# Kernel optimization log

Hardware: AMD Instinct MI355X
Metric: run time of the kernel (lower is better)

Reference implementation:

```python
import jax, jax.numpy as jnp
import numpy as np

EPS = 1e-5
GROUPS = 32

def group_norm(x, w, b):
    B, C, H, W = x.shape
    g = GROUPS
    xr = x.reshape(B, g, C // g, H * W)
    mean = xr.mean(axis=(2, 3), keepdims=True)
    var = xr.var(axis=(2, 3), keepdims=True)
    h = ((xr - mean) / jnp.sqrt(var + EPS)).reshape(B, C, H, W)
    return h * w[None, :, None, None] + b[None, :, None, None]

def setup_inputs() -> dict:
    key = jax.random.key(0)
    ks = jax.random.split(key, 7)
    B, C, H, W = 8, 256, 64, 64
    d = C // 8  # 32
    x = jax.random.normal(ks[0], (B, C, H, W), dtype=jnp.float32)
    norm_w = 1.0 + 0.1 * jax.random.normal(ks[1], (C,), dtype=jnp.float32)
    norm_b = 0.1 * jax.random.normal(ks[2], (C,), dtype=jnp.float32)
    s = 1.0 / np.sqrt(C)
    Wq = jax.random.normal(ks[3], (d, C), dtype=jnp.float32) * s
    Wk = jax.random.normal(ks[4], (d, C), dtype=jnp.float32) * s
    Wv = jax.random.normal(ks[5], (C, C), dtype=jnp.float32) * s
    Wproj = jax.random.normal(ks[6], (C, C), dtype=jnp.float32) * s
    gamma = jnp.full((1,), 0.5, dtype=jnp.float32)  # torch init is 0; nonzero so attention path contributes
    return {"x": x, "norm_w": norm_w, "norm_b": norm_b, "Wq": Wq, "Wk": Wk,
            "Wv": Wv, "Wproj": Wproj, "gamma": gamma}

def reference(x, norm_w, norm_b, Wq, Wk, Wv, Wproj, gamma):
    B, C, H, W = x.shape
    N = H * W
    h = group_norm(x, norm_w, norm_b)           # (B,C,H,W)
    hf = h.reshape(B, C, N)                      # flatten spatial
    d = Wq.shape[0]
    q = jnp.einsum('dc,bcn->bnd', Wq, hf)        # (B,N,d)
    k = jnp.einsum('dc,bcn->bdn', Wk, hf)        # (B,d,N)
    v = jnp.einsum('oc,bcn->bno', Wv, hf)        # (B,N,C)
    scale = d ** (-0.5)
    attn = jax.nn.softmax(jnp.einsum('bnd,bdm->bnm', q, k) * scale, axis=-1)  # (B,N,N)
    out = jnp.einsum('bnm,bmo->bno', attn, v)    # (B,N,C)
    out = out.transpose(0, 2, 1).reshape(B, C, H, W)
    proj = jnp.einsum('oc,bchw->bohw', Wproj, out)
    return x + gamma[0] * proj
```

## Files before the change

kernel.cpp:

```cpp
#include <hip/hip_runtime.h>
#include <cstdint>


typedef __bf16 bf16x8 __attribute__((ext_vector_type(8)));
typedef float f32x4 __attribute__((ext_vector_type(4)));
typedef float f32x16 __attribute__((ext_vector_type(16)));
typedef unsigned int u32x4 __attribute__((ext_vector_type(4)));
typedef unsigned short u16x4 __attribute__((ext_vector_type(4)));
typedef unsigned short u16x8 __attribute__((ext_vector_type(8)));

#define DEVI __device__ __forceinline__

DEVI unsigned short f2bf(float f) {
    __bf16 h = (__bf16)f;
    return __builtin_bit_cast(unsigned short, h);
}
DEVI float bf2f(unsigned short u) {
    unsigned int x = ((unsigned int)u) << 16;
    return __builtin_bit_cast(float, x);
}

DEVI f32x4 mfma16(bf16x8 a, bf16x8 b, f32x4 c) {
    return __builtin_amdgcn_mfma_f32_16x16x32_bf16(a, b, c, 0, 0, 0);
}
DEVI f32x16 mfma32(bf16x8 a, bf16x8 b, f32x16 c) {
    return __builtin_amdgcn_mfma_f32_32x32x16_bf16(a, b, c, 0, 0, 0);
}

DEVI void glds16(const unsigned short* g, unsigned short* l) {
    const __attribute__((address_space(1))) unsigned int* gp =
        reinterpret_cast<const __attribute__((address_space(1))) unsigned int*>(
            reinterpret_cast<uintptr_t>(g));
    __attribute__((address_space(3))) unsigned int* lp =
        reinterpret_cast<__attribute__((address_space(3))) unsigned int*>(
            reinterpret_cast<uintptr_t>(l));
    __builtin_amdgcn_global_load_lds(gp, lp, 16, 0, 0);
}

DEVI void barrier_raw() {
    asm volatile("" ::: "memory");
    __builtin_amdgcn_s_barrier();
    asm volatile("" ::: "memory");
}
DEVI void wait_vm0() {
    __builtin_amdgcn_s_waitcnt(0x3F70);
}

#define QSCALE 0.2550663133f
#define MFIX   12.0f

__global__ __launch_bounds__(1024) void k_gnorm(
        const float* __restrict__ x, const float* __restrict__ gw,
        const float* __restrict__ gb, unsigned short* __restrict__ ht) {
    int bg = blockIdx.x;
    int b = bg >> 5, g = bg & 31;
    const float* xb = x + ((size_t)(b * 256 + g * 8)) * 4096;
    int t = threadIdx.x;
    int n0 = t * 4;
    f32x4 cv[8];
    #pragma unroll
    for (int c = 0; c < 8; c++) cv[c] = *(const f32x4*)(xb + c * 4096 + n0);
    float s1 = 0.f, s2 = 0.f;
    #pragma unroll
    for (int c = 0; c < 8; c++) {
        #pragma unroll
        for (int j = 0; j < 4; j++) { s1 += cv[c][j]; s2 += cv[c][j] * cv[c][j]; }
    }
    #pragma unroll
    for (int off = 1; off < 64; off <<= 1) {
        s1 += __shfl_xor(s1, off);
        s2 += __shfl_xor(s2, off);
    }
    __shared__ float red[34];
    int wv_ = t >> 6;
    if ((t & 63) == 0) { red[wv_ * 2] = s1; red[wv_ * 2 + 1] = s2; }
    __syncthreads();
    if (t == 0) {
        float a = 0.f, q = 0.f;
        #pragma unroll
        for (int i = 0; i < 16; i++) { a += red[i * 2]; q += red[i * 2 + 1]; }
        float mean = a * (1.f / 32768.f);
        float var = q * (1.f / 32768.f) - mean * mean;
        red[32] = mean; red[33] = rsqrtf(var + 1e-5f);
    }
    __syncthreads();
    float mean = red[32], rstd = red[33];
    float wv8[8], bv8[8];
    #pragma unroll
    for (int c = 0; c < 8; c++) { wv8[c] = gw[g * 8 + c] * rstd; bv8[c] = gb[g * 8 + c] - mean * rstd * gw[g * 8 + c]; }
    #pragma unroll
    for (int j = 0; j < 4; j++) {
        u16x8 pk;
        #pragma unroll
        for (int c = 0; c < 8; c++) pk[c] = f2bf(cv[c][j] * wv8[c] + bv8[c]);
        *(u16x8*)(&ht[((size_t)(b * 4096 + n0 + j)) * 256 + g * 8]) = pk;
    }
}

template <int EPI>
__global__ __launch_bounds__(256) void k_gemm(
        const unsigned short* __restrict__ A, void* __restrict__ outp,
        const float* __restrict__ xres, const float* __restrict__ gamma, int ldout,
        const float* __restrict__ wqf, const float* __restrict__ wkf,
        const float* __restrict__ wvf, void* __restrict__ outp2) {
    __shared__ unsigned short lA[128 * 72];
    __shared__ unsigned short lB[64 * 72];
    int t = threadIdx.x;
    int m0 = blockIdx.x * 128, n0 = blockIdx.y * 64;
    if (EPI == 3) {
        if (blockIdx.y == 0) n0 = 0;
        else n0 = (blockIdx.y - 1) * 64;
    }
    int w = t >> 6, lane = t & 63, l15 = lane & 15, quad = lane >> 4;
    f32x4 z4 = {0.f, 0.f, 0.f, 0.f};
    f32x4 acc[2][4];
    #pragma unroll
    for (int i = 0; i < 2; i++)
        #pragma unroll
        for (int j = 0; j < 4; j++) acc[i][j] = z4;

    auto ldB8 = [&](int row, int gc) -> u16x8 {
        const float* src;
        float sc = 1.f;
        if (EPI == 3) {
            if (blockIdx.y == 0) {
                if (row < 32) { src = wqf + (size_t)row * 256 + gc; sc = QSCALE; }
                else          { src = wkf + (size_t)(row - 32) * 256 + gc; }
            } else {
                src = wvf + (size_t)(n0 + row) * 256 + gc;
            }
        } else {
            src = wvf + (size_t)(n0 + row) * 256 + gc;
        }
        f32x4 a = *(const f32x4*)src;
        f32x4 b2 = *(const f32x4*)(src + 4);
        u16x8 r;
        #pragma unroll
        for (int j = 0; j < 4; j++) { r[j] = f2bf(a[j] * sc); r[4 + j] = f2bf(b2[j] * sc); }
        return r;
    };

    for (int kb = 0; kb < 4; kb++) {
        #pragma unroll
        for (int i = 0; i < 4; i++) {
            int ch = i * 256 + t;
            int row = ch >> 3, col = (ch & 7) * 8;
            u32x4 v = *(const u32x4*)(A + (size_t)(m0 + row) * 256 + kb * 64 + col);
            *(u32x4*)(&lA[row * 72 + col]) = v;
        }
        #pragma unroll
        for (int i = 0; i < 2; i++) {
            int ch = i * 256 + t;
            int row = ch >> 3, col = (ch & 7) * 8;
            u16x8 v = ldB8(row, kb * 64 + col);
            *(u16x8*)(&lB[row * 72 + col]) = v;
        }
        __syncthreads();
        #pragma unroll
        for (int ks = 0; ks < 2; ks++) {
            bf16x8 af[2], bfr[4];
            #pragma unroll
            for (int fr = 0; fr < 2; fr++)
                af[fr] = *(const bf16x8*)(&lA[(w * 32 + fr * 16 + l15) * 72 + ks * 32 + quad * 8]);
            #pragma unroll
            for (int fn = 0; fn < 4; fn++)
                bfr[fn] = *(const bf16x8*)(&lB[(fn * 16 + l15) * 72 + ks * 32 + quad * 8]);
            #pragma unroll
            for (int fr = 0; fr < 2; fr++)
                #pragma unroll
                for (int fn = 0; fn < 4; fn++)
                    acc[fr][fn] = mfma16(af[fr], bfr[fn], acc[fr][fn]);
        }
        __syncthreads();
    }

    bool epi0 = (EPI == 3 && blockIdx.y == 0);
    bool epi1 = (EPI == 3 && blockIdx.y != 0);
    if (epi0) {
        unsigned short* out = (unsigned short*)outp;
        #pragma unroll
        for (int fr = 0; fr < 2; fr++)
            #pragma unroll
            for (int fn = 0; fn < 4; fn++)
                #pragma unroll
                for (int r = 0; r < 4; r++) {
                    int m = m0 + w * 32 + fr * 16 + quad * 4 + r;
                    int n = n0 + fn * 16 + l15;
                    out[(size_t)m * ldout + n] = f2bf(acc[fr][fn][r]);
                }
    } else if (epi1) {
        unsigned short* out = (unsigned short*)outp2;
        int b = m0 >> 12, nb = (m0 & 4095) + w * 32;
        int swq = ((quad & 1) << 1) | (quad >> 1);
        #pragma unroll
        for (int fr = 0; fr < 2; fr++)
            #pragma unroll
            for (int fn = 0; fn < 4; fn++) {
                int o = n0 + fn * 16 + l15;
                int n = nb + fr * 16 + swq * 4;
                u16x4 pk;
                #pragma unroll
                for (int r = 0; r < 4; r++) pk[r] = f2bf(acc[fr][fn][r]);
                *(u16x4*)(&out[(((size_t)(b * 256 + o)) << 12) + n]) = pk;
            }
    } else {
        float* out = (float*)outp;
        float gm = gamma[0];
        int b = m0 >> 12, nb = (m0 & 4095) + w * 32;
        #pragma unroll
        for (int fr = 0; fr < 2; fr++)
            #pragma unroll
            for (int fn = 0; fn < 4; fn++) {
                int o = n0 + fn * 16 + l15;
                int n = nb + fr * 16 + quad * 4;
                size_t base = (((size_t)(b * 256 + o)) << 12) + n;
                f32x4 xv = *(const f32x4*)(xres + base);
                f32x4 ov;
                #pragma unroll
                for (int r = 0; r < 4; r++) ov[r] = xv[r] + gm * acc[fr][fn][r];
                *(f32x4*)(out + base) = ov;
            }
    }
}

__global__ __launch_bounds__(256, 2) void k_flash(
        const unsigned short* __restrict__ QK, const unsigned short* __restrict__ Vt,
        unsigned short* __restrict__ Oa) {
    __shared__ __align__(16) char smem[40960];
    int id = blockIdx.x;
    int b = id & 7;
    int r3 = id >> 3;
    int oh = r3 & 1, qblk = r3 >> 1;
    int t = threadIdx.x, w = t >> 6, ln = t & 63;
    int l31 = ln & 31, h = ln >> 5;
    int qh = w >> 1, kh = w & 1;
    int q0 = qblk * 128 + qh * 64;

    bf16x8 qb0[2], qb1[2];
    #pragma unroll
    for (int qt2 = 0; qt2 < 2; qt2++) {
        const unsigned short* qrow = QK + ((size_t)(b * 4096 + q0 + qt2 * 32 + l31)) * 64;
        qb0[qt2] = *(const bf16x8*)(qrow + h * 8);
        qb1[qt2] = *(const bf16x8*)(qrow + 16 + h * 8);
    }

    int cgK = (ln & 3) ^ ((ln >> 2) & 3) ^ ((ln >> 4) & 3);
    const unsigned short* gK = QK + ((size_t)(b * 4096 + w * 16 + (ln >> 2))) * 64 + 32 + cgK * 8;
    int vc8 = (ln & 7) ^ ((ln >> 3) & 7);
    const unsigned short* gV = Vt + (((size_t)(b * 256 + oh * 128 + w * 32 + (ln >> 3))) << 12) + vc8 * 8;

    unsigned short* lK0 = (unsigned short*)smem;
    unsigned short* lV0 = (unsigned short*)(smem + 4096);
    unsigned short* lK1 = (unsigned short*)(smem + 20480);
    unsigned short* lV1 = (unsigned short*)(smem + 24576);
    unsigned short* sK0 = lK0 + w * 512;
    unsigned short* sV0 = lV0 + w * 2048;
    unsigned short* sK1 = lK1 + w * 512;
    unsigned short* sV1 = lV1 + w * 2048;

    f32x16 z16;
    #pragma unroll
    for (int i = 0; i < 16; i++) z16[i] = 0.f;
    f32x16 minit;
    #pragma unroll
    for (int i = 0; i < 16; i++) minit[i] = -MFIX;
    f32x16 Oacc[2][4];
    #pragma unroll
    for (int qt2 = 0; qt2 < 2; qt2++)
        #pragma unroll
        for (int i = 0; i < 4; i++) Oacc[qt2][i] = z16;
    float lsum[2] = {0.f, 0.f};

    int gl = (l31 & 3) ^ ((l31 >> 2) & 3);
    const unsigned short* kf0p0 = lK0 + (kh * 32 + l31) * 32 + ((0 + h) ^ gl) * 8;
    const unsigned short* kf1p0 = lK0 + (kh * 32 + l31) * 32 + ((2 + h) ^ gl) * 8;
    const unsigned short* kf0p1 = lK1 + (kh * 32 + l31) * 32 + ((0 + h) ^ gl) * 8;
    const unsigned short* kf1p1 = lK1 + (kh * 32 + l31) * 32 + ((2 + h) ^ gl) * 8;
    int slotA = ((kh * 4 + 0 * 2 + h) ^ (ln & 7)) * 8;
    int slotB = ((kh * 4 + 1 * 2 + h) ^ (ln & 7)) * 8;

    auto stage = [&](int kn, unsigned short* sK, unsigned short* sV) {
        glds16(gK + (size_t)kn * 4096, sK);
        #pragma unroll
        for (int j = 0; j < 4; j++)
            glds16(gV + ((size_t)j * 8 << 12) + kn * 64, sV + j * 512);
    };

    auto compute = [&](const unsigned short* kf0p, const unsigned short* kf1p,
                       const unsigned short* lV) {
        bf16x8 kf0 = *(const bf16x8*)kf0p;
        bf16x8 kf1 = *(const bf16x8*)kf1p;
        bf16x8 pa[2][2];
        #pragma unroll
        for (int qt2 = 0; qt2 < 2; qt2++) {
            f32x16 St = mfma32(kf0, qb0[qt2], minit);
            St = mfma32(kf1, qb1[qt2], St);
            u16x8 p0u, p1u;
            float s = 0.f;
            #pragma unroll
            for (int j = 0; j < 8; j++) {
                float e0 = __builtin_amdgcn_exp2f(St[j]);
                float e1 = __builtin_amdgcn_exp2f(St[8 + j]);
                s += e0 + e1;
                p0u[j] = f2bf(e0);
                p1u[j] = f2bf(e1);
            }
            lsum[qt2] += s;
            pa[qt2][0] = __builtin_bit_cast(bf16x8, p0u);
            pa[qt2][1] = __builtin_bit_cast(bf16x8, p1u);
        }
        __builtin_amdgcn_s_setprio(1);
        #pragma unroll
        for (int nt = 0; nt < 4; nt++) {
            bf16x8 vf = *(const bf16x8*)(lV + (nt * 32 + l31) * 64 + slotA);
            Oacc[0][nt] = mfma32(pa[0][0], vf, Oacc[0][nt]);
            Oacc[1][nt] = mfma32(pa[1][0], vf, Oacc[1][nt]);
        }
        #pragma unroll
        for (int nt = 0; nt < 4; nt++) {
            bf16x8 vf = *(const bf16x8*)(lV + (nt * 32 + l31) * 64 + slotB);
            Oacc[0][nt] = mfma32(pa[0][1], vf, Oacc[0][nt]);
            Oacc[1][nt] = mfma32(pa[1][1], vf, Oacc[1][nt]);
        }
        __builtin_amdgcn_s_setprio(0);
    };

    stage(0, sK0, sV0);
    for (int kt = 0; kt < 64; kt += 2) {
        wait_vm0();
        barrier_raw();
        stage(kt + 1, sK1, sV1);
        compute(kf0p0, kf1p0, lV0);
        wait_vm0();
        barrier_raw();
        if (kt + 2 < 64) stage(kt + 2, sK0, sV0);
        compute(kf0p1, kf1p1, lV1);
    }
    #pragma unroll
    for (int qt2 = 0; qt2 < 2; qt2++) lsum[qt2] += __shfl_xor(lsum[qt2], 32);
    __syncthreads();

    float* sf = (float*)smem;
    int lbase = (kh ? 8192 : 8320) + qh * 64 + l31;
    sf[lbase] = lsum[0];
    sf[lbase + 32] = lsum[1];
    if (kh == 1) {
        #pragma unroll
        for (int qt2 = 0; qt2 < 2; qt2++)
            #pragma unroll
            for (int nt = 0; nt < 4; nt++)
                #pragma unroll
                for (int rg = 0; rg < 2; rg++) {
                    u16x8 pk;
                    #pragma unroll
                    for (int j = 0; j < 8; j++) pk[j] = f2bf(Oacc[qt2][nt][rg * 8 + j]);
                    *(u16x8*)(smem + qh * 16384 + qt2 * 8192 + nt * 2048 + rg * 1024 + ln * 16) = pk;
                }
    }
    __syncthreads();
    if (kh == 0) {
        #pragma unroll
        for (int qt2 = 0; qt2 < 2; qt2++) {
            float rl[16];
            #pragma unroll
            for (int r = 0; r < 16; r++) {
                int row = (r & 3) + 8 * (r >> 2) + 4 * h;
                float l = sf[8192 + qh * 64 + qt2 * 32 + row] +
                          sf[8320 + qh * 64 + qt2 * 32 + row];
                rl[r] = 1.f / l;
            }
            size_t rb = (size_t)(b * 4096 + qblk * 128 + qh * 64 + qt2 * 32);
            #pragma unroll
            for (int nt = 0; nt < 4; nt++)
                #pragma unroll
                for (int rg = 0; rg < 2; rg++) {
                    u16x8 pk = *(const u16x8*)(smem + qh * 16384 + qt2 * 8192 + nt * 2048 + rg * 1024 + ln * 16);
                    #pragma unroll
                    for (int j = 0; j < 8; j++) {
                        int r = rg * 8 + j;
                        float val = (Oacc[qt2][nt][r] + bf2f(pk[j])) * rl[r];
                        int row = (r & 3) + 8 * (r >> 2) + 4 * h;
                        Oa[(rb + row) * 256 + oh * 128 + nt * 32 + l31] = f2bf(val);
                    }
                }
        }
    }
}

extern "C" void kernel_launch(void* const* d_in, const int* in_sizes, int n_in,
                              void* d_out, int out_size, void* d_ws, size_t ws_size,
                              hipStream_t stream) {
    const float* x  = (const float*)d_in[0];
    const float* nw = (const float*)d_in[1];
    const float* nb = (const float*)d_in[2];
    const float* wq = (const float*)d_in[3];
    const float* wk = (const float*)d_in[4];
    const float* wv = (const float*)d_in[5];
    const float* wp = (const float*)d_in[6];
    const float* gm = (const float*)d_in[7];

    char* p = (char*)d_ws;
    unsigned short* ht  = (unsigned short*)p; p += (size_t)32768 * 256 * 2;
    unsigned short* qk  = (unsigned short*)p; p += (size_t)32768 * 64 * 2;
    unsigned short* vt  = (unsigned short*)p; p += (size_t)8 * 256 * 4096 * 2;
    unsigned short* oa  = (unsigned short*)p; p += (size_t)32768 * 256 * 2;

    k_gnorm<<<dim3(256), dim3(1024), 0, stream>>>(x, nw, nb, ht);
    k_gemm<3><<<dim3(256, 5), dim3(256), 0, stream>>>(ht, (void*)qk, nullptr, nullptr, 64, wq, wk, wv, (void*)vt);
    k_flash<<<dim3(512), dim3(256), 0, stream>>>(qk, vt, oa);
    k_gemm<2><<<dim3(256, 4), dim3(256), 0, stream>>>(oa, d_out, x, gm, 0, nullptr, nullptr, wp, nullptr);
}
```

Measured before the change: 225.3 us.

## Retile flash kernel to cover all output channels per block with fewer query rows

The flash-attention kernel previously split the 256 value channels across two blocks, each handling 128 query rows, so QK^T and the exp for each key tile were computed twice. Each block now covers all 256 output channels for 64 query rows, so the score and softmax work per key is done once. The cost is that each block stages twice as much V per tile in shared memory (which grows to 72KB), and per-block K loads are repeated across more blocks. This may reduce occupancy at the launch bound of 2 blocks per CU.

```diff
diff --git a/kernel.cpp b/kernel.cpp
--- a/kernel.cpp
+++ b/kernel.cpp
@@ -226,37 +226,31 @@
 __global__ __launch_bounds__(256, 2) void k_flash(
         const unsigned short* __restrict__ QK, const unsigned short* __restrict__ Vt,
         unsigned short* __restrict__ Oa) {
-    __shared__ __align__(16) char smem[40960];
+    __shared__ __align__(16) char smem[73728];
     int id = blockIdx.x;
     int b = id & 7;
-    int r3 = id >> 3;
-    int oh = r3 & 1, qblk = r3 >> 1;
+    int qblk = id >> 3;
     int t = threadIdx.x, w = t >> 6, ln = t & 63;
     int l31 = ln & 31, h = ln >> 5;
     int qh = w >> 1, kh = w & 1;
-    int q0 = qblk * 128 + qh * 64;
-
-    bf16x8 qb0[2], qb1[2];
-    #pragma unroll
-    for (int qt2 = 0; qt2 < 2; qt2++) {
-        const unsigned short* qrow = QK + ((size_t)(b * 4096 + q0 + qt2 * 32 + l31)) * 64;
-        qb0[qt2] = *(const bf16x8*)(qrow + h * 8);
-        qb1[qt2] = *(const bf16x8*)(qrow + 16 + h * 8);
-    }
+
+    const unsigned short* qrow = QK + ((size_t)(b * 4096 + qblk * 64 + qh * 32 + l31)) * 64;
+    bf16x8 qb0 = *(const bf16x8*)(qrow + h * 8);
+    bf16x8 qb1 = *(const bf16x8*)(qrow + 16 + h * 8);
 
     int cgK = (ln & 3) ^ ((ln >> 2) & 3) ^ ((ln >> 4) & 3);
     const unsigned short* gK = QK + ((size_t)(b * 4096 + w * 16 + (ln >> 2))) * 64 + 32 + cgK * 8;
     int vc8 = (ln & 7) ^ ((ln >> 3) & 7);
-    const unsigned short* gV = Vt + (((size_t)(b * 256 + oh * 128 + w * 32 + (ln >> 3))) << 12) + vc8 * 8;
+    const unsigned short* gV = Vt + (((size_t)(b * 256 + w * 64 + (ln >> 3))) << 12) + vc8 * 8;
 
     unsigned short* lK0 = (unsigned short*)smem;
     unsigned short* lV0 = (unsigned short*)(smem + 4096);
-    unsigned short* lK1 = (unsigned short*)(smem + 20480);
-    unsigned short* lV1 = (unsigned short*)(smem + 24576);
+    unsigned short* lK1 = (unsigned short*)(smem + 36864);
+    unsigned short* lV1 = (unsigned short*)(smem + 40960);
     unsigned short* sK0 = lK0 + w * 512;
-    unsigned short* sV0 = lV0 + w * 2048;
+    unsigned short* sV0 = lV0 + w * 4096;
     unsigned short* sK1 = lK1 + w * 512;
-    unsigned short* sV1 = lV1 + w * 2048;
+    unsigned short* sV1 = lV1 + w * 4096;
 
     f32x16 z16;
     #pragma unroll
@@ -264,12 +258,10 @@
     f32x16 minit;
     #pragma unroll
     for (int i = 0; i < 16; i++) minit[i] = -MFIX;
-    f32x16 Oacc[2][4];
-    #pragma unroll
-    for (int qt2 = 0; qt2 < 2; qt2++)
-        #pragma unroll
-        for (int i = 0; i < 4; i++) Oacc[qt2][i] = z16;
-    float lsum[2] = {0.f, 0.f};
+    f32x16 Oacc[8];
+    #pragma unroll
+    for (int i = 0; i < 8; i++) Oacc[i] = z16;
+    float lsum = 0.f;
 
     int gl = (l31 & 3) ^ ((l31 >> 2) & 3);
     const unsigned short* kf0p0 = lK0 + (kh * 32 + l31) * 32 + ((0 + h) ^ gl) * 8;
@@ -282,7 +274,7 @@
     auto stage = [&](int kn, unsigned short* sK, unsigned short* sV) {
         glds16(gK + (size_t)kn * 4096, sK);
         #pragma unroll
-        for (int j = 0; j < 4; j++)
+        for (int j = 0; j < 8; j++)
             glds16(gV + ((size_t)j * 8 << 12) + kn * 64, sV + j * 512);
     };
 
@@ -290,37 +282,31 @@
                        const unsigned short* lV) {
         bf16x8 kf0 = *(const bf16x8*)kf0p;
         bf16x8 kf1 = *(const bf16x8*)kf1p;
-        bf16x8 pa[2][2];
-        #pragma unroll
-        for (int qt2 = 0; qt2 < 2; qt2++) {
-            f32x16 St = mfma32(kf0, qb0[qt2], minit);
-            St = mfma32(kf1, qb1[qt2], St);
-            u16x8 p0u, p1u;
-            float s = 0.f;
-            #pragma unroll
-            for (int j = 0; j < 8; j++) {
-                float e0 = __builtin_amdgcn_exp2f(St[j]);
-                float e1 = __builtin_amdgcn_exp2f(St[8 + j]);
-                s += e0 + e1;
-                p0u[j] = f2bf(e0);
-                p1u[j] = f2bf(e1);
-            }
-            lsum[qt2] += s;
-            pa[qt2][0] = __builtin_bit_cast(bf16x8, p0u);
-            pa[qt2][1] = __builtin_bit_cast(bf16x8, p1u);
-        }
+        f32x16 St = mfma32(kf0, qb0, minit);
+        St = mfma32(kf1, qb1, St);
+        u16x8 p0u, p1u;
+        float s = 0.f;
+        #pragma unroll
+        for (int j = 0; j < 8; j++) {
+            float e0 = __builtin_amdgcn_exp2f(St[j]);
+            float e1 = __builtin_amdgcn_exp2f(St[8 + j]);
+            s += e0 + e1;
+            p0u[j] = f2bf(e0);
+            p1u[j] = f2bf(e1);
+        }
+        lsum += s;
+        bf16x8 pa0 = __builtin_bit_cast(bf16x8, p0u);
+        bf16x8 pa1 = __builtin_bit_cast(bf16x8, p1u);
         __builtin_amdgcn_s_setprio(1);
         #pragma unroll
-        for (int nt = 0; nt < 4; nt++) {
-            bf16x8 vf = *(const bf16x8*)(lV + (nt * 32 + l31) * 64 + slotA);
-            Oacc[0][nt] = mfma32(pa[0][0], vf, Oacc[0][nt]);
-            Oacc[1][nt] = mfma32(pa[1][0], vf, Oacc[1][nt]);
-        }
-        #pragma unroll
-        for (int nt = 0; nt < 4; nt++) {
-            bf16x8 vf = *(const bf16x8*)(lV + (nt * 32 + l31) * 64 + slotB);
-            Oacc[0][nt] = mfma32(pa[0][1], vf, Oacc[0][nt]);
-            Oacc[1][nt] = mfma32(pa[1][1], vf, Oacc[1][nt]);
+        for (int ot = 0; ot < 8; ot++) {
+            bf16x8 vf = *(const bf16x8*)(lV + (ot * 32 + l31) * 64 + slotA);
+            Oacc[ot] = mfma32(pa0, vf, Oacc[ot]);
+        }
+        #pragma unroll
+        for (int ot = 0; ot < 8; ot++) {
+            bf16x8 vf = *(const bf16x8*)(lV + (ot * 32 + l31) * 64 + slotB);
+            Oacc[ot] = mfma32(pa1, vf, Oacc[ot]);
         }
         __builtin_amdgcn_s_setprio(0);
     };
@@ -336,54 +322,46 @@
         if (kt + 2 < 64) stage(kt + 2, sK0, sV0);
         compute(kf0p1, kf1p1, lV1);
     }
-    #pragma unroll
-    for (int qt2 = 0; qt2 < 2; qt2++) lsum[qt2] += __shfl_xor(lsum[qt2], 32);
+    lsum += __shfl_xor(lsum, 32);
     __syncthreads();
 
     float* sf = (float*)smem;
-    int lbase = (kh ? 8192 : 8320) + qh * 64 + l31;
-    sf[lbase] = lsum[0];
-    sf[lbase + 32] = lsum[1];
+    int lbase = (kh ? 8192 : 8256) + qh * 32 + l31;
+    sf[lbase] = lsum;
     if (kh == 1) {
         #pragma unroll
-        for (int qt2 = 0; qt2 < 2; qt2++)
-            #pragma unroll
-            for (int nt = 0; nt < 4; nt++)
-                #pragma unroll
-                for (int rg = 0; rg < 2; rg++) {
-                    u16x8 pk;
-                    #pragma unroll
-                    for (int j = 0; j < 8; j++) pk[j] = f2bf(Oacc[qt2][nt][rg * 8 + j]);
-                    *(u16x8*)(smem + qh * 16384 + qt2 * 8192 + nt * 2048 + rg * 1024 + ln * 16) = pk;
-                }
+        for (int ot = 0; ot < 8; ot++)
+            #pragma unroll
+            for (int rg = 0; rg < 2; rg++) {
+                u16x8 pk;
+                #pragma unroll
+                for (int j = 0; j < 8; j++) pk[j] = f2bf(Oacc[ot][rg * 8 + j]);
+                *(u16x8*)(smem + qh * 16384 + ot * 2048 + rg * 1024 + ln * 16) = pk;
+            }
     }
     __syncthreads();
     if (kh == 0) {
-        #pragma unroll
-        for (int qt2 = 0; qt2 < 2; qt2++) {
-            float rl[16];
-            #pragma unroll
-            for (int r = 0; r < 16; r++) {
-                int row = (r & 3) + 8 * (r >> 2) + 4 * h;
-                float l = sf[8192 + qh * 64 + qt2 * 32 + row] +
-                          sf[8320 + qh * 64 + qt2 * 32 + row];
-                rl[r] = 1.f / l;
-            }
-            size_t rb = (size_t)(b * 4096 + qblk * 128 + qh * 64 + qt2 * 32);
-            #pragma unroll
-            for (int nt = 0; nt < 4; nt++)
-                #pragma unroll
-                for (int rg = 0; rg < 2; rg++) {
-                    u16x8 pk = *(const u16x8*)(smem + qh * 16384 + qt2 * 8192 + nt * 2048 + rg * 1024 + ln * 16);
-                    #pragma unroll
-                    for (int j = 0; j < 8; j++) {
-                        int r = rg * 8 + j;
-                        float val = (Oacc[qt2][nt][r] + bf2f(pk[j])) * rl[r];
-                        int row = (r & 3) + 8 * (r >> 2) + 4 * h;
-                        Oa[(rb + row) * 256 + oh * 128 + nt * 32 + l31] = f2bf(val);
-                    }
+        float rl[16];
+        #pragma unroll
+        for (int r = 0; r < 16; r++) {
+            int row = (r & 3) + 8 * (r >> 2) + 4 * h;
+            float l = sf[8192 + qh * 32 + row] + sf[8256 + qh * 32 + row];
+            rl[r] = 1.f / l;
+        }
+        size_t rb = (size_t)(b * 4096 + qblk * 64 + qh * 32);
+        #pragma unroll
+        for (int ot = 0; ot < 8; ot++)
+            #pragma unroll
+            for (int rg = 0; rg < 2; rg++) {
+                u16x8 pk = *(const u16x8*)(smem + qh * 16384 + ot * 2048 + rg * 1024 + ln * 16);
+                #pragma unroll
+                for (int j = 0; j < 8; j++) {
+                    int r = rg * 8 + j;
+                    float val = (Oacc[ot][r] + bf2f(pk[j])) * rl[r];
+                    int row = (r & 3) + 8 * (r >> 2) + 4 * h;
+                    Oa[(rb + row) * 256 + ot * 32 + l31] = f2bf(val);
                 }
-        }
+            }
     }
 }
 
```

Result: slower. 230.0 us (+2.1%).
